# Performance work log

Hardware: AMD Instinct MI355X
Metric: run time of the kernel (lower is better)

## Reference

```python
import jax, jax.numpy as jnp
from jax import lax
import numpy as np


def setup_inputs() -> dict:
    key = jax.random.key(0)
    ks = iter(jax.random.split(key, 48))

    def w(shape):
        fan = shape[0] if len(shape) == 2 else int(np.prod(shape[1:]))
        return jax.random.normal(next(ks), shape, jnp.float32) / np.sqrt(fan)

    def b(n):
        return jax.random.normal(next(ks), (n,), jnp.float32) * 0.01

    T = 16
    return dict(
        search=jax.random.normal(next(ks), (3, 383, 287), jnp.float32),
        exemplars=jax.random.normal(next(ks), (T, 3, 383, 287), jnp.float32),
        # AlexNet features (random-weight stand-in for pretrained)
        aw1=w((64, 3, 11, 11)), ab1=b(64),
        aw2=w((192, 64, 5, 5)), ab2=b(192),
        aw3=w((384, 192, 3, 3)), ab3=b(384),
        aw4=w((256, 384, 3, 3)), ab4=b(256),
        aw5=w((256, 256, 3, 3)), ab5=b(256),
        # conv_deconv: Conv1d(256,256,3,p=1) -> MaxPool1d(88) -> ConvTranspose1d(256,256,88)
        wcd=w((256, 256, 3)), bcd=b(256),
        wt=w((256, 256, 88)), bt=b(256),
        # st_gcn: GCN(256, 512, 256)
        ws1=w((256, 512)), bs1=b(512),
        ws2=w((512, 256)), bs2=b(256),
        # g, h: 1x1 Conv1d(256,256) == linear maps
        wg=w((256, 256)), bg=b(256),
        wh=w((256, 256)), bh=b(256),
        # ct_gcn: GCN(256, 384, 256)
        wc1=w((256, 384)), bc1=b(384),
        wc2=w((384, 256)), bc2=b(256),
    )


def _gct_forward(search, exemplars, aw1, ab1, aw2, ab2, aw3, ab3, aw4, ab4,
                 aw5, ab5, wcd, bcd, wt, bt, ws1, bs1, ws2, bs2,
                 wg, bg, wh, bh, wc1, bc1, wc2, bc2):
    f32 = jnp.float32

    def conv2d(x, w, bias, s, p):
        y = lax.conv_general_dilated(x, w, (s, s), [(p, p), (p, p)],
                                     dimension_numbers=('NCHW', 'OIHW', 'NCHW'))
        return y + bias[None, :, None, None]

    def maxpool(x):  # k=3, s=2, VALID (AlexNet pools)
        return lax.reduce_window(x, -jnp.inf, lax.max, (1, 1, 3, 3), (1, 1, 2, 2), 'VALID')

    def features(x):
        x = maxpool(jax.nn.relu(conv2d(x, aw1, ab1, 4, 2)))
        x = maxpool(jax.nn.relu(conv2d(x, aw2, ab2, 1, 2)))
        x = jax.nn.relu(conv2d(x, aw3, ab3, 1, 1))
        x = jax.nn.relu(conv2d(x, aw4, ab4, 1, 1))
        x = maxpool(jax.nn.relu(conv2d(x, aw5, ab5, 1, 1)))
        return x

    lrelu = lambda v: jax.nn.leaky_relu(v, 0.01)

    X = features(search[None])          # [1,256,11,8]
    Z = features(exemplars)             # [T,256,11,8]
    T = Z.shape[0]
    D = X.shape[1]                      # 256
    M = X.shape[2] * X.shape[3]         # 88
    Xf = X.reshape(D, M)                # [256,88]
    Zf = Z.reshape(T, D, M)             # [T,256,88]

    # conv_deconv branch: conv1d(k=3,p=1) -> global maxpool -> conv_transpose(k=M)
    xc = lax.conv_general_dilated(Xf[None], wcd, (1,), [(1, 1)],
                                  dimension_numbers=('NCH', 'OIH', 'NCH'))[0] + bcd[:, None]
    v = jnp.max(xc, axis=1)                              # [256]
    X_hat = jnp.einsum('i,iok->ok', v, wt) + bt[:, None]  # [256,88]

    # spatiotemporal graph: A[i+T*j, i+T*k]=1 for j!=k; self-loops for t!=0
    TM = T * M
    n = jnp.arange(TM)
    same_t = (n[:, None] % T) == (n[None, :] % T)
    diff_s = (n[:, None] // T) != (n[None, :] // T)
    A1 = (same_t & diff_s).astype(f32) + jnp.diag((n % T != 0).astype(f32))

    # st GCN over TM nodes (node n = t + T*m -> spatial-major flatten)
    nodes = Zf.transpose(2, 0, 1).reshape(TM, D)          # [TM,256]
    h1 = lrelu(A1 @ (nodes @ ws1) + bs1)                  # [TM,512]
    h2 = lrelu(A1 @ (h1 @ ws2) + bs2)                     # [TM,256]
    V1 = jnp.max(h2.reshape(M, T, D), axis=1).T           # temporal max-pool -> [256,88]

    # dynamic cross-track graph: pairwise g/h affinities + row softmax (fused)
    Vx = V1 + X_hat                                       # [256,88]
    G = wg @ Vx + bg[:, None]                             # [256,88]
    Hh = wh @ Vx + bh[:, None]                            # [256,88]
    A2 = jax.nn.softmax(Hh.T @ G, axis=1)                 # [88,88], A2[j,i]=g(i).h(j)

    # ct GCN
    xv = V1.T                                             # [88,256]
    c1 = lrelu(A2 @ (xv @ wc1) + bc1)                     # [88,384]
    V2 = lrelu(A2 @ (c1 @ wc2) + bc2).T                   # [256,88]

    # F.conv2d(X[1,256,11,8], V2[1,256,11,8]) -> full-overlap correlation = scalar
    R = jnp.sum(Xf * V2).reshape(1, 1, 1, 1)
    return R


def reference(search, exemplars, aw1, ab1, aw2, ab2, aw3, ab3, aw4, ab4,
              aw5, ab5, wcd, bcd, wt, bt, ws1, bs1, ws2, bs2,
              wg, bg, wh, bh, wc1, bc1, wc2, bc2):
    return _gct_forward(search, exemplars, aw1, ab1, aw2, ab2, aw3, ab3, aw4, ab4,
                        aw5, ab5, wcd, bcd, wt, bt, ws1, bs1, ws2, bs2,
                        wg, bg, wh, bh, wc1, bc1, wc2, bc2)
```

## Files before the change

kernel.cpp:

```cpp
#include <hip/hip_runtime.h>
#include <hip/hip_bf16.h>
#include <math.h>

#define BATCH 17
#define T_EX 16
#define H0 383
#define W0 287
#define C1 64
#define H1 95
#define W1 71
#define H1P 47
#define W1P 35
#define C2 192
#define H2P 23
#define W2P 17
#define C3 384
#define C45 256
#define H5P 11
#define W5P 8
#define DD 256
#define MM 88
#define TM 1408

#define HP1 389
#define WP1 292

typedef unsigned short ushort_t;
typedef __attribute__((ext_vector_type(8))) short short8;
typedef __attribute__((ext_vector_type(4))) float f32x4;

__device__ __forceinline__ float lrelu(float v) { return v > 0.f ? v : 0.01f * v; }

__device__ __forceinline__ ushort_t f2bf(float f) {
    unsigned int u = __float_as_uint(f);
    unsigned int r = (u + 0x7fffu + ((u >> 16) & 1u)) >> 16;
    return (ushort_t)r;
}
__device__ __forceinline__ float b2f(ushort_t b) {
    return __uint_as_float(((unsigned int)b) << 16);
}
__device__ __forceinline__ short8 ld16(const ushort_t* p) { return *(const short8*)p; }
__device__ __forceinline__ short8 ld2x8(const ushort_t* p) {
    union { uint2 u[2]; short8 s; } uu;
    uu.u[0] = *(const uint2*)p;
    uu.u[1] = *(const uint2*)(p + 4);
    return uu.s;
}
__device__ __forceinline__ void async_cp16(ushort_t* l, const ushort_t* g) {
    __builtin_amdgcn_global_load_lds(
        (const __attribute__((address_space(1))) void*)g,
        (__attribute__((address_space(3))) void*)l, 16, 0, 0);
}

__global__ void zfill_k(float4* __restrict__ p, int n4) {
    int idx = blockIdx.x * 256 + threadIdx.x;
    if (idx < n4) p[idx] = (float4){0.f, 0.f, 0.f, 0.f};
}

__global__ void prep1_k(const float* __restrict__ search, const float* __restrict__ exemp,
                        ushort_t* __restrict__ out) {
    int idx = blockIdx.x * 256 + threadIdx.x;
    if (idx >= BATCH * H0 * W0) return;
    int ix = idx % W0; int t = idx / W0;
    int iy = t % H0; int b = t / H0;
    const float* src = (b == 0) ? search : exemp + (size_t)(b - 1) * 3 * H0 * W0;
    const int hw = H0 * W0;
    float v0 = src[iy * W0 + ix];
    float v1 = src[hw + iy * W0 + ix];
    float v2 = src[2 * hw + iy * W0 + ix];
    ushort4 o;
    o.x = f2bf(v0); o.y = f2bf(v1); o.z = f2bf(v2); o.w = 0;
    *(ushort4*)&out[(((size_t)b * HP1 + iy + 2) * WP1 + ix + 2) * 4] = o;
}

__global__ void wprep_k(const float* __restrict__ w, ushort_t* __restrict__ out,
                        int KH, int KWl, int KWr, int CINl, int CINr,
                        int NKS, int nch, int OCr) {
    int idx = blockIdx.x * 256 + threadIdx.x;
    if (idx >= nch) return;
    int c = idx & 255;
    int rest = idx >> 8;
    int ks = rest % NKS;
    int ocb = rest / NKS;
    int k8 = c >> 6, m = c & 63;
    int oc = ocb * 64 + m;
    int KWC = KWl * CINl;
    ushort_t* o = out + (size_t)idx * 8;
#pragma unroll
    for (int j = 0; j < 8; ++j) {
        int kg = ks * 32 + k8 * 8 + j;
        int ky = kg / KWC; int rem = kg - ky * KWC;
        int kx = rem / CINl; int ic = rem - kx * CINl;
        float v = 0.f;
        if (oc < OCr && ky < KH && kx < KWr && ic < CINr)
            v = w[(((size_t)oc * CINr + ic) * KH + ky) * KWr + kx];
        o[j] = f2bf(v);
    }
}

__global__ void wprep_gemm_k(const float* __restrict__ ws1, const float* __restrict__ ws2,
                             const float* __restrict__ wcd, ushort_t* __restrict__ WS1T,
                             ushort_t* __restrict__ WS2T, ushort_t* __restrict__ WCDT) {
    int idx = blockIdx.x * 256 + threadIdx.x;
    const float* src; ushort_t* dst; int NKS, mode = 0, sa = 1, sk = 0, base;
    if (idx < 16384)       { src = ws1; dst = WS1T; NKS = 8;  sk = 512; base = idx; }
    else if (idx < 32768)  { src = ws2; dst = WS2T; NKS = 16; sk = 256; base = idx - 16384; }
    else if (idx < 57344)  { src = wcd; dst = WCDT; NKS = 24; mode = 1; base = idx - 32768; }
    else return;
    int c = base & 255;
    int rest = base >> 8;
    int ks = rest % NKS;
    int ocb = rest / NKS;
    int k8 = c >> 6, m = c & 63;
    int oc = ocb * 64 + m;
    ushort_t* o = dst + (size_t)base * 8;
#pragma unroll
    for (int j = 0; j < 8; ++j) {
        int kg = ks * 32 + k8 * 8 + j;
        float v;
        if (mode == 0) v = src[(size_t)oc * sa + (size_t)kg * sk];
        else           v = src[(size_t)oc * 768 + (kg & 255) * 3 + (kg >> 8)];
        o[j] = f2bf(v);
    }
}

template <int STRIDE, bool A16>
__global__ __launch_bounds__(256) void conv_mfma13(
    const ushort_t* __restrict__ inp, const ushort_t* __restrict__ wt,
    const float* __restrict__ bias, ushort_t* __restrict__ out,
    int Hp, int Wp, int C, int Wout, int HW, int NKS2, int KWl,
    int OHp, int OWp, int OPAD, int COUT) {
    const int tid = threadIdx.x;
    const int wv = tid >> 6, lane = tid & 63;
    const int quad = lane >> 4, l16 = lane & 15;
    const int n_blk = blockIdx.x * 64;
    const int ocb = blockIdx.y;
    const int b = blockIdx.z;

    __shared__ ushort_t As[2][4096];
    __shared__ ushort_t Bs[2][4096];
    __shared__ int offs[432];

    const int KWC = KWl * C;
    for (int g = tid; g < NKS2 * 8; g += 256) {
        int kg = g * 8;
        int ky = kg / KWC; int rem = kg - ky * KWC;
        int kx = rem / C; int c8 = rem - kx * C;
        offs[g] = (ky * Wp + kx) * C + c8;
    }

    const ushort_t* inb = inp + (size_t)b * Hp * Wp * C;

    const int g8 = lane & 7, po = lane >> 3;
    int np0 = n_blk + wv * 16 + po;      if (np0 >= HW) np0 = HW - 1;
    int np1 = n_blk + wv * 16 + 8 + po;  if (np1 >= HW) np1 = HW - 1;
    const ushort_t* bsrc0;
    const ushort_t* bsrc1;
    {
        int oy0 = np0 / Wout, ox0 = np0 - oy0 * Wout;
        int oy1 = np1 / Wout, ox1 = np1 - oy1 * Wout;
        bsrc0 = inb + (size_t)(oy0 * STRIDE * Wp + ox0 * STRIDE) * C;
        bsrc1 = inb + (size_t)(oy1 * STRIDE * Wp + ox1 * STRIDE) * C;
    }
    const int ws0 = g8 * 512 + (((wv * 16 + po) ^ g8) * 8);
    const int ws1 = g8 * 512 + (((wv * 16 + 8 + po) ^ g8) * 8);

    int n_g = n_blk + lane;
    int n_gc = n_g < HW ? n_g : HW - 1;
    int oyl = n_gc / Wout, oxl = n_gc - oyl * Wout;
    const int base0 = (oyl * STRIDE * Wp + oxl * STRIDE) * C;

    f32x4 acc[4];
#pragma unroll
    for (int cn = 0; cn < 4; ++cn) acc[cn] = (f32x4){0.f, 0.f, 0.f, 0.f};

    const ushort_t* wblk = wt + (size_t)ocb * (size_t)NKS2 * 4096;

    __syncthreads();

    {
        const ushort_t* aS = wblk + tid * 8;
        async_cp16(&As[0][tid * 8], aS);
        async_cp16(&As[0][2048 + tid * 8], aS + 2048);
        if constexpr (A16) {
            short8 r0v = ld16(bsrc0 + offs[g8]);
            short8 r1v = ld16(bsrc1 + offs[g8]);
            *(short8*)&Bs[0][ws0] = r0v;
            *(short8*)&Bs[0][ws1] = r1v;
        } else {
            const int o0 = offs[wv], o1 = offs[4 + wv];
            *(short8*)&Bs[0][tid * 8] = ld2x8(inb + base0 + o0);
            *(short8*)&Bs[0][2048 + tid * 8] = ld2x8(inb + base0 + o1);
        }
    }
    __syncthreads();

    for (int ks2 = 0; ks2 < NKS2; ++ks2) {
        const int cur = ks2 & 1, nxt = cur ^ 1;
        const bool more = (ks2 + 1 < NKS2);
        short8 rb0, rb1;
        if (more) {
            const ushort_t* aS = wblk + (size_t)(ks2 + 1) * 4096 + tid * 8;
            async_cp16(&As[nxt][tid * 8], aS);
            async_cp16(&As[nxt][2048 + tid * 8], aS + 2048);
            if constexpr (A16) {
                rb0 = ld16(bsrc0 + offs[(ks2 + 1) * 8 + g8]);
                rb1 = ld16(bsrc1 + offs[(ks2 + 1) * 8 + g8]);
            } else {
                const int o0 = offs[(ks2 + 1) * 8 + wv], o1 = offs[(ks2 + 1) * 8 + 4 + wv];
                *(short8*)&Bs[nxt][tid * 8] = ld2x8(inb + base0 + o0);
                *(short8*)&Bs[nxt][2048 + tid * 8] = ld2x8(inb + base0 + o1);
            }
        }
#pragma unroll
        for (int h = 0; h < 2; ++h) {
            const short8 af = *(const short8*)&As[cur][h * 2048 + (quad * 64 + wv * 16 + l16) * 8];
#pragma unroll
            for (int cn = 0; cn < 4; ++cn) {
                int bidx;
                if constexpr (A16)
                    bidx = h * 2048 + quad * 512 + (((cn * 16 + l16) ^ (h * 4 + quad)) * 8);
                else
                    bidx = h * 2048 + (quad * 64 + cn * 16 + l16) * 8;
                const short8 bfr = *(const short8*)&Bs[cur][bidx];
                acc[cn] = __builtin_amdgcn_mfma_f32_16x16x32_bf16(af, bfr, acc[cn], 0, 0, 0);
            }
        }
        if constexpr (A16) {
            if (more) {
                *(short8*)&Bs[nxt][ws0] = rb0;
                *(short8*)&Bs[nxt][ws1] = rb1;
            }
        }
        __syncthreads();
    }

    const int oc0 = ocb * 64 + wv * 16 + quad * 4;
    const float bi0 = bias[oc0], bi1 = bias[oc0 + 1], bi2 = bias[oc0 + 2], bi3 = bias[oc0 + 3];
#pragma unroll
    for (int cn = 0; cn < 4; ++cn) {
        int n = n_blk + cn * 16 + l16;
        if (n < HW) {
            int y = n / Wout, x = n - y * Wout;
            size_t base = (((size_t)b * OHp + y + OPAD) * OWp + x + OPAD) * COUT + oc0;
            ushort4 o;
            o.x = f2bf(fmaxf(acc[cn][0] + bi0, 0.f));
            o.y = f2bf(fmaxf(acc[cn][1] + bi1, 0.f));
            o.z = f2bf(fmaxf(acc[cn][2] + bi2, 0.f));
            o.w = f2bf(fmaxf(acc[cn][3] + bi3, 0.f));
            *(ushort4*)&out[base] = o;
        }
    }
}

template <int MODE, bool HASBIAS, bool SC1>
__global__ __launch_bounds__(256) void gemm_mfma3(
    const ushort_t* __restrict__ Bsrc, const ushort_t* __restrict__ wt,
    const float* __restrict__ bias, float* __restrict__ out,
    int RS, int N, int NKS, int sn, int sc) {
    const int tid = threadIdx.x;
    const int wv = tid >> 6, lane = tid & 63;
    const int quad = lane >> 4, l16 = lane & 15;
    const int n_blk = blockIdx.x * 64;
    const int ocb = blockIdx.y;

    __shared__ ushort_t Bs[2][2048];

    int n_g = n_blk + lane;
    int n_gc = n_g < N ? n_g : N - 1;
    int row = (MODE == 1) ? (1 + (n_gc & 15)) * MM + (n_gc >> 4) : n_gc;
    const size_t base0 = (size_t)row * RS;

    f32x4 acc[4];
#pragma unroll
    for (int cn = 0; cn < 4; ++cn) acc[cn] = (f32x4){0.f, 0.f, 0.f, 0.f};

    const ushort_t* wblk = wt + (size_t)ocb * NKS * 2048;
    const int afrag = (quad * 64 + wv * 16 + l16) * 8;

    short8 a0 = ld16(wblk + afrag);
    *(short8*)&Bs[0][tid * 8] = ld16(Bsrc + base0 + wv * 8);
    __syncthreads();

    for (int ks = 0; ks < NKS; ++ks) {
        const int cur = ks & 1, nxt = cur ^ 1;
        short8 a1, bn;
        const bool more = (ks + 1 < NKS);
        if (more) {
            a1 = ld16(wblk + (ks + 1) * 2048 + afrag);
            bn = ld16(Bsrc + base0 + (ks + 1) * 32 + wv * 8);
        }
#pragma unroll
        for (int cn = 0; cn < 4; ++cn) {
            const short8 bfr = *(const short8*)&Bs[cur][(quad * 64 + cn * 16 + l16) * 8];
            acc[cn] = __builtin_amdgcn_mfma_f32_16x16x32_bf16(a0, bfr, acc[cn], 0, 0, 0);
        }
        if (more) *(short8*)&Bs[nxt][tid * 8] = bn;
        a0 = a1;
        __syncthreads();
    }

    const int oc0 = ocb * 64 + wv * 16 + quad * 4;
    float bb[4] = {0.f, 0.f, 0.f, 0.f};
    if (HASBIAS) { bb[0] = bias[oc0]; bb[1] = bias[oc0+1]; bb[2] = bias[oc0+2]; bb[3] = bias[oc0+3]; }
#pragma unroll
    for (int cn = 0; cn < 4; ++cn) {
        int n = n_blk + cn * 16 + l16;
        if (n < N) {
            if (SC1) {
                float4 o;
                o.x = acc[cn][0] + bb[0]; o.y = acc[cn][1] + bb[1];
                o.z = acc[cn][2] + bb[2]; o.w = acc[cn][3] + bb[3];
                *(float4*)&out[(size_t)n * sn + oc0] = o;
            } else {
#pragma unroll
                for (int reg = 0; reg < 4; ++reg)
                    out[(size_t)n * sn + (size_t)(oc0 + reg) * sc] = acc[cn][reg] + bb[reg];
            }
        }
    }
}

__global__ void pool_nhwc(const ushort_t* __restrict__ in, ushort_t* __restrict__ out,
                          int C, int Hin, int Win, int Hout, int Wout,
                          int OHp, int OWp, int OPAD) {
    int total = BATCH * C * Hout * Wout;
    int idx = blockIdx.x * 256 + threadIdx.x;
    if (idx >= total) return;
    int c = idx % C; int r = idx / C;
    int x = r % Wout; r /= Wout;
    int y = r % Hout; int b = r / Hout;
    const int rs = Win * C;
    const ushort_t* p = in + (((size_t)b * Hin + 2 * y) * Win + 2 * x) * C + c;
    float m = b2f(p[0]);
    m = fmaxf(m, b2f(p[C])); m = fmaxf(m, b2f(p[2 * C]));
    m = fmaxf(m, b2f(p[rs])); m = fmaxf(m, b2f(p[rs + C])); m = fmaxf(m, b2f(p[rs + 2 * C]));
    m = fmaxf(m, b2f(p[2 * rs])); m = fmaxf(m, b2f(p[2 * rs + C])); m = fmaxf(m, b2f(p[2 * rs + 2 * C]));
    out[(((size_t)b * OHp + y + OPAD) * OWp + x + OPAD) * C + c] = f2bf(m);
}

__global__ void pool5_k(const ushort_t* __restrict__ in, float* __restrict__ P,
                        ushort_t* __restrict__ PB, ushort_t* __restrict__ XfPad) {
    int total = BATCH * 256 * MM;
    int idx = blockIdx.x * 256 + threadIdx.x;
    if (idx >= total) return;
    int c = idx % 256; int r = idx / 256;
    int x = r % W5P; r /= W5P;
    int y = r % H5P; int b = r / H5P;
    const int rs = W2P * 256;
    const ushort_t* p = in + (((size_t)b * H2P + 2 * y) * W2P + 2 * x) * 256 + c;
    float m = b2f(p[0]);
    m = fmaxf(m, b2f(p[256])); m = fmaxf(m, b2f(p[512]));
    m = fmaxf(m, b2f(p[rs])); m = fmaxf(m, b2f(p[rs + 256])); m = fmaxf(m, b2f(p[rs + 512]));
    m = fmaxf(m, b2f(p[2 * rs])); m = fmaxf(m, b2f(p[2 * rs + 256])); m = fmaxf(m, b2f(p[2 * rs + 512]));
    int mm = y * W5P + x;
    size_t o = ((size_t)b * MM + mm) * 256 + c;
    P[o] = m;
    ushort_t mb = f2bf(m);
    PB[o] = mb;
    if (b == 0) XfPad[(size_t)(mm + 1) * 256 + c] = mb;
}

__global__ void xhat2_k(const float* __restrict__ xc, const float* __restrict__ wt,
                        const float* __restrict__ bt, float* __restrict__ xhat) {
    __shared__ float lv[256];
    {
        int j = threadIdx.x;
        const float* xr = xc + (size_t)j * MM;
        float mx = xr[0];
        for (int k = 1; k < MM; ++k) mx = fmaxf(mx, xr[k]);
        lv[j] = mx;
    }
    __syncthreads();
    int idx = blockIdx.x * 256 + threadIdx.x;
    if (idx >= DD * MM) return;
    int k = idx % MM, o = idx / MM;
    float acc = bt[o];
    for (int i = 0; i < 256; ++i) acc = fmaf(lv[i], wt[(i * 256 + o) * MM + k], acc);
    xhat[idx] = acc;
}

__global__ void sh1_k(const float* __restrict__ Y1, const float* __restrict__ bs1,
                      ushort_t* __restrict__ h1b) {
    int idx = blockIdx.x * 256 + threadIdx.x;
    if (idx >= T_EX * 512) return;
    int c = idx & 511, t = idx >> 9;
    float s = 0.f;
    for (int m = 0; m < MM; ++m) s += Y1[(size_t)(m * T_EX + t) * 512 + c];
    float base = s + bs1[c];
    if (t == 0) {
        for (int m = 0; m < MM; ++m) {
            float val = base - Y1[(size_t)(m * T_EX) * 512 + c];
            h1b[(size_t)(m * T_EX) * 512 + c] = f2bf(lrelu(val));
        }
    } else {
        ushort_t v = f2bf(lrelu(base));
        for (int m = 0; m < MM; ++m)
            h1b[(size_t)(m * T_EX + t) * 512 + c] = v;
    }
}

__global__ void sh2_k(const float* __restrict__ Y2, const float* __restrict__ bs2,
                      float* __restrict__ h2) {
    int idx = blockIdx.x * 256 + threadIdx.x;
    if (idx >= T_EX * 256) return;
    int c = idx & 255, t = idx >> 8;
    float s = 0.f;
    for (int m = 0; m < MM; ++m) s += Y2[(size_t)(m * T_EX + t) * 256 + c];
    float base = s + bs2[c];
    if (t == 0) {
        for (int m = 0; m < MM; ++m)
            h2[(size_t)(m * T_EX) * 256 + c] = lrelu(base - Y2[(size_t)(m * T_EX) * 256 + c]);
    } else {
        float v = lrelu(base);
        for (int m = 0; m < MM; ++m) h2[(size_t)(m * T_EX + t) * 256 + c] = v;
    }
}

__global__ void v1vx_k(const float* __restrict__ h2, const float* __restrict__ xhat,
                       float* __restrict__ V1, float* __restrict__ Vx) {
    int idx = blockIdx.x * 256 + threadIdx.x;
    if (idx >= DD * MM) return;
    int m = idx % MM, d = idx / MM;
    float mx = -INFINITY;
    for (int t = 0; t < T_EX; ++t) mx = fmaxf(mx, h2[(m * T_EX + t) * 256 + d]);
    V1[idx] = mx;
    Vx[idx] = mx + xhat[idx];
}

__global__ void lin88_k(const float* __restrict__ Wg, const float* __restrict__ bg,
                        const float* __restrict__ Wh, const float* __restrict__ bh,
                        const float* __restrict__ Vin, float* __restrict__ Gout,
                        float* __restrict__ Hout) {
    int idx = blockIdx.x * 256 + threadIdx.x;
    if (idx >= DD * MM) return;
    const float* W = blockIdx.y ? Wh : Wg;
    const float* bias = blockIdx.y ? bh : bg;
    float* out = blockIdx.y ? Hout : Gout;
    int m = idx % MM, o = idx / MM;
    const float* wr = W + o * 256;
    float acc = bias[o];
    for (int i = 0; i < 256; ++i) acc = fmaf(wr[i], Vin[i * MM + m], acc);
    out[idx] = acc;
}

__global__ void smsm_k(const float* __restrict__ Hh, const float* __restrict__ G,
                       float* __restrict__ A2) {
    int j = blockIdx.x;
    int tid = threadIdx.x;
    __shared__ float row[96];
    __shared__ float red[128];
    for (int i = tid; i < MM; i += 128) {
        float acc = 0.f;
        for (int c = 0; c < 256; ++c) acc = fmaf(Hh[c * MM + j], G[c * MM + i], acc);
        row[i] = acc;
    }
    __syncthreads();
    float val = (tid < MM) ? row[tid] : -INFINITY;
    red[tid] = val; __syncthreads();
    for (int s = 64; s > 0; s >>= 1) {
        if (tid < s) red[tid] = fmaxf(red[tid], red[tid + s]);
        __syncthreads();
    }
    float mx = red[0]; __syncthreads();
    float e = (tid < MM) ? expf(val - mx) : 0.f;
    red[tid] = e; __syncthreads();
    for (int s = 64; s > 0; s >>= 1) {
        if (tid < s) red[tid] += red[tid + s];
        __syncthreads();
    }
    float inv = 1.f / red[0];
    if (tid < MM) A2[j * MM + tid] = e * inv;
}

__global__ void t1_k(const float* __restrict__ V1, const float* __restrict__ wc1,
                     float* __restrict__ t1) {
    int idx = blockIdx.x * 256 + threadIdx.x;
    if (idx >= MM * 384) return;
    int c = idx % 384, m = idx / 384;
    float acc = 0.f;
    for (int d = 0; d < 256; ++d) acc = fmaf(V1[d * MM + m], wc1[d * 384 + c], acc);
    t1[idx] = acc;
}

__global__ void c1_k(const float* __restrict__ A2, const float* __restrict__ t1,
                     const float* __restrict__ bc1, float* __restrict__ c1) {
    int idx = blockIdx.x * 256 + threadIdx.x;
    if (idx >= MM * 384) return;
    int c = idx % 384, j = idx / 384;
    float acc = bc1[c];
    for (int i = 0; i < MM; ++i) acc = fmaf(A2[j * MM + i], t1[i * 384 + c], acc);
    c1[idx] = lrelu(acc);
}

__global__ void t2_k(const float* __restrict__ c1, const float* __restrict__ wc2,
                     float* __restrict__ t2) {
    int idx = blockIdx.x * 256 + threadIdx.x;
    if (idx >= MM * 256) return;
    int c = idx % 256, m = idx / 256;
    const float* cr = c1 + m * 384;
    float acc = 0.f;
    for (int d = 0; d < 384; ++d) acc = fmaf(cr[d], wc2[d * 256 + c], acc);
    t2[idx] = acc;
}

__global__ void v2_k(const float* __restrict__ A2, const float* __restrict__ t2,
                     const float* __restrict__ bc2, float* __restrict__ V2m) {
    int idx = blockIdx.x * 256 + threadIdx.x;
    if (idx >= MM * 256) return;
    int c = idx % 256, j = idx / 256;
    float acc = bc2[c];
    for (int i = 0; i < MM; ++i) acc = fmaf(A2[j * MM + i], t2[i * 256 + c], acc);
    V2m[idx] = lrelu(acc);
}

__global__ void final_k(const float* __restrict__ Xf2, const float* __restrict__ V2m,
                        float* __restrict__ out) {
    __shared__ float red[256];
    float acc = 0.f;
    for (int idx = threadIdx.x; idx < DD * MM; idx += 256)
        acc = fmaf(Xf2[idx], V2m[idx], acc);
    red[threadIdx.x] = acc; __syncthreads();
    for (int s = 128; s > 0; s >>= 1) {
        if (threadIdx.x < s) red[threadIdx.x] += red[threadIdx.x + s];
        __syncthreads();
    }
    if (threadIdx.x == 0) out[0] = red[0];
}

extern "C" void kernel_launch(void* const* d_in, const int* in_sizes, int n_in,
                              void* d_out, int out_size, void* d_ws, size_t ws_size,
                              hipStream_t stream) {
    const float* search = (const float*)d_in[0];
    const float* exemp  = (const float*)d_in[1];
    const float* aw1 = (const float*)d_in[2];  const float* ab1 = (const float*)d_in[3];
    const float* aw2 = (const float*)d_in[4];  const float* ab2 = (const float*)d_in[5];
    const float* aw3 = (const float*)d_in[6];  const float* ab3 = (const float*)d_in[7];
    const float* aw4 = (const float*)d_in[8];  const float* ab4 = (const float*)d_in[9];
    const float* aw5 = (const float*)d_in[10]; const float* ab5 = (const float*)d_in[11];
    const float* wcd = (const float*)d_in[12]; const float* bcd = (const float*)d_in[13];
    const float* wt  = (const float*)d_in[14]; const float* bt  = (const float*)d_in[15];
    const float* ws1 = (const float*)d_in[16]; const float* bs1 = (const float*)d_in[17];
    const float* ws2 = (const float*)d_in[18]; const float* bs2 = (const float*)d_in[19];
    const float* wg  = (const float*)d_in[20]; const float* bg  = (const float*)d_in[21];
    const float* wh  = (const float*)d_in[22]; const float* bh  = (const float*)d_in[23];
    const float* wc1 = (const float*)d_in[24]; const float* bc1 = (const float*)d_in[25];
    const float* wc2 = (const float*)d_in[26]; const float* bc2 = (const float*)d_in[27];

    float* ws = (float*)d_ws;
    float* R1 = ws;
    float* R2 = ws + 3870720;
    float* R3 = ws + 7544832;
    float* Wg = ws + 8628864;

    ushort_t* in1p  = (ushort_t*)R1;
    ushort_t* c1out = (ushort_t*)R2;
    ushort_t* p1out = (ushort_t*)R3;
    ushort_t* c2out = (ushort_t*)R1;
    ushort_t* p2out = (ushort_t*)R2;
    ushort_t* c3out = (ushort_t*)(R2 + 775200);
    ushort_t* c4out = (ushort_t*)R1;
    ushort_t* c5out = (ushort_t*)R3;
    ushort_t* WT    = (ushort_t*)Wg;

    zfill_k<<<(965500 + 255) / 256, 256, 0, stream>>>((float4*)R1, 965500);
    prep1_k<<<(BATCH * H0 * W0 + 255) / 256, 256, 0, stream>>>(search, exemp, in1p);
    wprep_k<<<(4608 + 255) / 256, 256, 0, stream>>>(aw1, WT, 11, 12, 11, 4, 3, 18, 4608, 64);
    conv_mfma13<4, false><<<dim3(106, 1, BATCH), 256, 0, stream>>>(
        in1p, WT, ab1, c1out, HP1, WP1, 4, W1, H1 * W1, 9, 12, H1, W1, 0, 64);
    zfill_k<<<(270504 + 255) / 256, 256, 0, stream>>>((float4*)R3, 270504);
    pool_nhwc<<<(BATCH * 64 * H1P * W1P + 255) / 256, 256, 0, stream>>>(
        c1out, p1out, 64, H1, W1, H1P, W1P, 51, 39, 2);
    wprep_k<<<(38400 + 255) / 256, 256, 0, stream>>>(aw2, WT, 5, 5, 5, 64, 64, 50, 38400, 192);
    conv_mfma13<1, true><<<dim3(26, 3, BATCH), 256, 0, stream>>>(
        p1out, WT, ab2, c2out, 51, 39, 64, W1P, H1P * W1P, 25, 5, H1P, W1P, 0, 192);
    zfill_k<<<(581400 + 255) / 256, 256, 0, stream>>>((float4*)R2, 581400);
    pool_nhwc<<<(BATCH * 192 * H2P * W2P + 255) / 256, 256, 0, stream>>>(
        c2out, p2out, 192, H1P, W1P, H2P, W2P, 25, 19, 1);
    wprep_k<<<(82944 + 255) / 256, 256, 0, stream>>>(aw3, WT, 3, 3, 3, 192, 192, 54, 82944, 384);
    conv_mfma13<1, true><<<dim3(7, 6, BATCH), 256, 0, stream>>>(
        p2out, WT, ab3, c3out, 25, 19, 192, W2P, H2P * W2P, 27, 3, 25, 19, 1, 384);
    zfill_k<<<(258400 + 255) / 256, 256, 0, stream>>>((float4*)R1, 258400);
    wprep_k<<<(110592 + 255) / 256, 256, 0, stream>>>(aw4, WT, 3, 3, 3, 384, 384, 108, 110592, 256);
    conv_mfma13<1, true><<<dim3(7, 4, BATCH), 256, 0, stream>>>(
        c3out, WT, ab4, c4out, 25, 19, 384, W2P, H2P * W2P, 54, 3, 25, 19, 1, 256);
    wprep_k<<<(73728 + 255) / 256, 256, 0, stream>>>(aw5, WT, 3, 3, 3, 256, 256, 72, 73728, 256);
    conv_mfma13<1, true><<<dim3(7, 4, BATCH), 256, 0, stream>>>(
        c4out, WT, ab5, c5out, 25, 19, 256, W2P, H2P * W2P, 36, 3, H2P, W2P, 0, 256);

    float*    P      = R1 + 2417664;
    ushort_t* PB     = (ushort_t*)(R1 + 2800640);
    ushort_t* XfPad  = (ushort_t*)(R1 + 2992128);
    float*    xc     = R1 + 3003648;

    ushort_t* WS1T = (ushort_t*)Wg;
    ushort_t* WS2T = (ushort_t*)(Wg + 65536);
    ushort_t* WCDT = (ushort_t*)(Wg + 131072);
    wprep_gemm_k<<<(57344 + 255) / 256, 256, 0, stream>>>(ws1, ws2, wcd, WS1T, WS2T, WCDT);

    pool5_k<<<(BATCH * 256 * MM + 255) / 256, 256, 0, stream>>>(c5out, P, PB, XfPad);
    float* Xf2 = P;

    float* xhat = R1 + 1024;
    float* Y1   = R1 + 23552;
    ushort_t* h1b = (ushort_t*)(R1 + 752640);
    float* Y2   = R1 + 1473536;
    float* h2   = R1 + 1838080;
    float* V1   = R1 + 2198528;
    float* Vx   = R1 + 2221056;
    float* G    = R1 + 2243584;
    float* Hh   = R1 + 2266112;
    float* A2   = R1 + 2296832;
    float* t1   = R1 + 2305024;
    float* c1   = R1 + 2338816;
    float* t2   = R1 + 2372608;
    float* V2m  = R1 + 2395136;

    gemm_mfma3<0, true, false><<<dim3(2, 4), 256, 0, stream>>>(
        XfPad, WCDT, bcd, xc, 256, MM, 24, 1, MM);
    xhat2_k<<<(DD * MM + 255) / 256, 256, 0, stream>>>(xc, wt, bt, xhat);

    gemm_mfma3<1, false, true><<<dim3(22, 8), 256, 0, stream>>>(
        PB, WS1T, nullptr, Y1, 256, TM, 8, 512, 1);
    sh1_k<<<(T_EX * 512 + 255) / 256, 256, 0, stream>>>(Y1, bs1, h1b);
    gemm_mfma3<0, false, true><<<dim3(22, 4), 256, 0, stream>>>(
        h1b, WS2T, nullptr, Y2, 512, TM, 16, 256, 1);
    sh2_k<<<(T_EX * 256 + 255) / 256, 256, 0, stream>>>(Y2, bs2, h2);
    v1vx_k<<<(DD * MM + 255) / 256, 256, 0, stream>>>(h2, xhat, V1, Vx);

    lin88_k<<<dim3((DD * MM + 255) / 256, 2), 256, 0, stream>>>(wg, bg, wh, bh, Vx, G, Hh);
    smsm_k<<<MM, 128, 0, stream>>>(Hh, G, A2);

    t1_k<<<(MM * 384 + 255) / 256, 256, 0, stream>>>(V1, wc1, t1);
    c1_k<<<(MM * 384 + 255) / 256, 256, 0, stream>>>(A2, t1, bc1, c1);
    t2_k<<<(MM * 256 + 255) / 256, 256, 0, stream>>>(c1, wc2, t2);
    v2_k<<<(MM * 256 + 255) / 256, 256, 0, stream>>>(A2, t2, bc2, V2m);

    final_k<<<1, 256, 0, stream>>>(Xf2, V2m, (float*)d_out);
}
```

Measured before the change: 548.2 us.

## Fold batch into conv N dimension, 2x2 wave tiling, and merge small kernels

The conv kernel now flattens batch and pixels into one N dimension, so tiles no longer waste work on per-image remainders, and each wave computes a 32x32 output sub-tile with 2x2 MFMAs instead of 16x64. Zero-fill passes are removed: the input prep writes its own padding, and the remaining fills are folded into pool and weight-prep launches. Several small GEMM and elementwise kernels are merged into combined launches (gemm pair, xhat+sh1, lin+t1, wprep+pool5). This cuts launch count and idle tile work, at the cost of more divergent multi-role kernels and different register pressure.

```diff
diff --git a/kernel.cpp b/kernel.cpp
--- a/kernel.cpp
+++ b/kernel.cpp
@@ -52,30 +52,34 @@
         (__attribute__((address_space(3))) void*)l, 16, 0, 0);
 }
 
-__global__ void zfill_k(float4* __restrict__ p, int n4) {
-    int idx = blockIdx.x * 256 + threadIdx.x;
-    if (idx < n4) p[idx] = (float4){0.f, 0.f, 0.f, 0.f};
-}
-
-__global__ void prep1_k(const float* __restrict__ search, const float* __restrict__ exemp,
-                        ushort_t* __restrict__ out) {
-    int idx = blockIdx.x * 256 + threadIdx.x;
-    if (idx >= BATCH * H0 * W0) return;
-    int ix = idx % W0; int t = idx / W0;
-    int iy = t % H0; int b = t / H0;
-    const float* src = (b == 0) ? search : exemp + (size_t)(b - 1) * 3 * H0 * W0;
-    const int hw = H0 * W0;
-    float v0 = src[iy * W0 + ix];
-    float v1 = src[hw + iy * W0 + ix];
-    float v2 = src[2 * hw + iy * W0 + ix];
-    ushort4 o;
-    o.x = f2bf(v0); o.y = f2bf(v1); o.z = f2bf(v2); o.w = 0;
-    *(ushort4*)&out[(((size_t)b * HP1 + iy + 2) * WP1 + ix + 2) * 4] = o;
+__global__ void prep1f_k(const float* __restrict__ search, const float* __restrict__ exemp,
+                         ushort_t* __restrict__ out) {
+    int idx = blockIdx.x * 256 + threadIdx.x;
+    if (idx >= BATCH * HP1 * WP1) return;
+    int x = idx % WP1; int t = idx / WP1;
+    int y = t % HP1; int b = t / HP1;
+    ushort4 o = {0, 0, 0, 0};
+    int ix = x - 2, iy = y - 2;
+    if (ix >= 0 && ix < W0 && iy >= 0 && iy < H0) {
+        const float* src = (b == 0) ? search : exemp + (size_t)(b - 1) * 3 * H0 * W0;
+        const int hw = H0 * W0;
+        o.x = f2bf(src[iy * W0 + ix]);
+        o.y = f2bf(src[hw + iy * W0 + ix]);
+        o.z = f2bf(src[2 * hw + iy * W0 + ix]);
+    }
+    *(ushort4*)&out[(size_t)idx * 4] = o;
 }
 
 __global__ void wprep_k(const float* __restrict__ w, ushort_t* __restrict__ out,
                         int KH, int KWl, int KWr, int CINl, int CINr,
-                        int NKS, int nch, int OCr) {
+                        int NKS, int nch, int OCr,
+                        float4* __restrict__ zp, int zn4) {
+    const int wb = (nch + 255) >> 8;
+    if ((int)blockIdx.x >= wb) {
+        int z = (blockIdx.x - wb) * 256 + threadIdx.x;
+        if (z < zn4) zp[z] = (float4){0.f, 0.f, 0.f, 0.f};
+        return;
+    }
     int idx = blockIdx.x * 256 + threadIdx.x;
     if (idx >= nch) return;
     int c = idx & 255;
@@ -98,44 +102,18 @@
     }
 }
 
-__global__ void wprep_gemm_k(const float* __restrict__ ws1, const float* __restrict__ ws2,
-                             const float* __restrict__ wcd, ushort_t* __restrict__ WS1T,
-                             ushort_t* __restrict__ WS2T, ushort_t* __restrict__ WCDT) {
-    int idx = blockIdx.x * 256 + threadIdx.x;
-    const float* src; ushort_t* dst; int NKS, mode = 0, sa = 1, sk = 0, base;
-    if (idx < 16384)       { src = ws1; dst = WS1T; NKS = 8;  sk = 512; base = idx; }
-    else if (idx < 32768)  { src = ws2; dst = WS2T; NKS = 16; sk = 256; base = idx - 16384; }
-    else if (idx < 57344)  { src = wcd; dst = WCDT; NKS = 24; mode = 1; base = idx - 32768; }
-    else return;
-    int c = base & 255;
-    int rest = base >> 8;
-    int ks = rest % NKS;
-    int ocb = rest / NKS;
-    int k8 = c >> 6, m = c & 63;
-    int oc = ocb * 64 + m;
-    ushort_t* o = dst + (size_t)base * 8;
-#pragma unroll
-    for (int j = 0; j < 8; ++j) {
-        int kg = ks * 32 + k8 * 8 + j;
-        float v;
-        if (mode == 0) v = src[(size_t)oc * sa + (size_t)kg * sk];
-        else           v = src[(size_t)oc * 768 + (kg & 255) * 3 + (kg >> 8)];
-        o[j] = f2bf(v);
-    }
-}
-
 template <int STRIDE, bool A16>
-__global__ __launch_bounds__(256) void conv_mfma13(
+__global__ __launch_bounds__(256) void conv_mfma14(
     const ushort_t* __restrict__ inp, const ushort_t* __restrict__ wt,
     const float* __restrict__ bias, ushort_t* __restrict__ out,
-    int Hp, int Wp, int C, int Wout, int HW, int NKS2, int KWl,
+    int Hp, int Wp, int C, int Wout, int HW, int Ntot, int NKS2, int KWl,
     int OHp, int OWp, int OPAD, int COUT) {
     const int tid = threadIdx.x;
     const int wv = tid >> 6, lane = tid & 63;
     const int quad = lane >> 4, l16 = lane & 15;
+    const int wr = wv >> 1, wc = wv & 1;
     const int n_blk = blockIdx.x * 64;
     const int ocb = blockIdx.y;
-    const int b = blockIdx.z;
 
     __shared__ ushort_t As[2][4096];
     __shared__ ushort_t Bs[2][4096];
@@ -149,30 +127,35 @@
         offs[g] = (ky * Wp + kx) * C + c8;
     }
 
-    const ushort_t* inb = inp + (size_t)b * Hp * Wp * C;
+    const size_t HWC = (size_t)Hp * Wp * C;
 
     const int g8 = lane & 7, po = lane >> 3;
-    int np0 = n_blk + wv * 16 + po;      if (np0 >= HW) np0 = HW - 1;
-    int np1 = n_blk + wv * 16 + 8 + po;  if (np1 >= HW) np1 = HW - 1;
-    const ushort_t* bsrc0;
-    const ushort_t* bsrc1;
-    {
-        int oy0 = np0 / Wout, ox0 = np0 - oy0 * Wout;
-        int oy1 = np1 / Wout, ox1 = np1 - oy1 * Wout;
-        bsrc0 = inb + (size_t)(oy0 * STRIDE * Wp + ox0 * STRIDE) * C;
-        bsrc1 = inb + (size_t)(oy1 * STRIDE * Wp + ox1 * STRIDE) * C;
-    }
-    const int ws0 = g8 * 512 + (((wv * 16 + po) ^ g8) * 8);
-    const int ws1 = g8 * 512 + (((wv * 16 + 8 + po) ^ g8) * 8);
-
-    int n_g = n_blk + lane;
-    int n_gc = n_g < HW ? n_g : HW - 1;
-    int oyl = n_gc / Wout, oxl = n_gc - oyl * Wout;
-    const int base0 = (oyl * STRIDE * Wp + oxl * STRIDE) * C;
-
-    f32x4 acc[4];
-#pragma unroll
-    for (int cn = 0; cn < 4; ++cn) acc[cn] = (f32x4){0.f, 0.f, 0.f, 0.f};
+    const ushort_t* bsrc0 = nullptr; const ushort_t* bsrc1 = nullptr;
+    const ushort_t* lsrc = nullptr;
+    int ws0 = 0, ws1 = 0;
+    if constexpr (A16) {
+        int np0 = n_blk + wv * 16 + po;      if (np0 >= Ntot) np0 = Ntot - 1;
+        int np1 = n_blk + wv * 16 + 8 + po;  if (np1 >= Ntot) np1 = Ntot - 1;
+        int b0 = np0 / HW, p0 = np0 - b0 * HW;
+        int b1 = np1 / HW, p1 = np1 - b1 * HW;
+        int oy0 = p0 / Wout, ox0 = p0 - oy0 * Wout;
+        int oy1 = p1 / Wout, ox1 = p1 - oy1 * Wout;
+        bsrc0 = inp + (size_t)b0 * HWC + (size_t)(oy0 * STRIDE * Wp + ox0 * STRIDE) * C;
+        bsrc1 = inp + (size_t)b1 * HWC + (size_t)(oy1 * STRIDE * Wp + ox1 * STRIDE) * C;
+        ws0 = g8 * 512 + (((wv * 16 + po) ^ g8) * 8);
+        ws1 = g8 * 512 + (((wv * 16 + 8 + po) ^ g8) * 8);
+    } else {
+        int n0 = n_blk + lane; if (n0 >= Ntot) n0 = Ntot - 1;
+        int b0 = n0 / HW, p0 = n0 - b0 * HW;
+        int oy = p0 / Wout, ox = p0 - oy * Wout;
+        lsrc = inp + (size_t)b0 * HWC + (size_t)(oy * STRIDE * Wp + ox * STRIDE) * C;
+    }
+
+    f32x4 acc[2][2];
+#pragma unroll
+    for (int am = 0; am < 2; ++am)
+#pragma unroll
+        for (int bn = 0; bn < 2; ++bn) acc[am][bn] = (f32x4){0.f, 0.f, 0.f, 0.f};
 
     const ushort_t* wblk = wt + (size_t)ocb * (size_t)NKS2 * 4096;
 
@@ -183,14 +166,12 @@
         async_cp16(&As[0][tid * 8], aS);
         async_cp16(&As[0][2048 + tid * 8], aS + 2048);
         if constexpr (A16) {
-            short8 r0v = ld16(bsrc0 + offs[g8]);
-            short8 r1v = ld16(bsrc1 + offs[g8]);
-            *(short8*)&Bs[0][ws0] = r0v;
-            *(short8*)&Bs[0][ws1] = r1v;
+            *(short8*)&Bs[0][ws0] = ld16(bsrc0 + offs[g8]);
+            *(short8*)&Bs[0][ws1] = ld16(bsrc1 + offs[g8]);
         } else {
             const int o0 = offs[wv], o1 = offs[4 + wv];
-            *(short8*)&Bs[0][tid * 8] = ld2x8(inb + base0 + o0);
-            *(short8*)&Bs[0][2048 + tid * 8] = ld2x8(inb + base0 + o1);
+            *(short8*)&Bs[0][tid * 8] = ld2x8(lsrc + o0);
+            *(short8*)&Bs[0][2048 + tid * 8] = ld2x8(lsrc + o1);
         }
     }
     __syncthreads();
@@ -208,23 +189,26 @@
                 rb1 = ld16(bsrc1 + offs[(ks2 + 1) * 8 + g8]);
             } else {
                 const int o0 = offs[(ks2 + 1) * 8 + wv], o1 = offs[(ks2 + 1) * 8 + 4 + wv];
-                *(short8*)&Bs[nxt][tid * 8] = ld2x8(inb + base0 + o0);
-                *(short8*)&Bs[nxt][2048 + tid * 8] = ld2x8(inb + base0 + o1);
+                *(short8*)&Bs[nxt][tid * 8] = ld2x8(lsrc + o0);
+                *(short8*)&Bs[nxt][2048 + tid * 8] = ld2x8(lsrc + o1);
             }
         }
 #pragma unroll
         for (int h = 0; h < 2; ++h) {
-            const short8 af = *(const short8*)&As[cur][h * 2048 + (quad * 64 + wv * 16 + l16) * 8];
-#pragma unroll
-            for (int cn = 0; cn < 4; ++cn) {
-                int bidx;
-                if constexpr (A16)
-                    bidx = h * 2048 + quad * 512 + (((cn * 16 + l16) ^ (h * 4 + quad)) * 8);
-                else
-                    bidx = h * 2048 + (quad * 64 + cn * 16 + l16) * 8;
-                const short8 bfr = *(const short8*)&Bs[cur][bidx];
-                acc[cn] = __builtin_amdgcn_mfma_f32_16x16x32_bf16(af, bfr, acc[cn], 0, 0, 0);
+            const short8 a0 = *(const short8*)&As[cur][h * 2048 + (quad * 64 + wr * 32 + l16) * 8];
+            const short8 a1 = *(const short8*)&As[cur][h * 2048 + (quad * 64 + wr * 32 + 16 + l16) * 8];
+            short8 b0, b1;
+            if constexpr (A16) {
+                b0 = *(const short8*)&Bs[cur][h * 2048 + quad * 512 + (((wc * 32 + l16) ^ (h * 4 + quad)) * 8)];
+                b1 = *(const short8*)&Bs[cur][h * 2048 + quad * 512 + (((wc * 32 + 16 + l16) ^ (h * 4 + quad)) * 8)];
+            } else {
+                b0 = *(const short8*)&Bs[cur][h * 2048 + (quad * 64 + wc * 32 + l16) * 8];
+                b1 = *(const short8*)&Bs[cur][h * 2048 + (quad * 64 + wc * 32 + 16 + l16) * 8];
             }
+            acc[0][0] = __builtin_amdgcn_mfma_f32_16x16x32_bf16(a0, b0, acc[0][0], 0, 0, 0);
+            acc[0][1] = __builtin_amdgcn_mfma_f32_16x16x32_bf16(a0, b1, acc[0][1], 0, 0, 0);
+            acc[1][0] = __builtin_amdgcn_mfma_f32_16x16x32_bf16(a1, b0, acc[1][0], 0, 0, 0);
+            acc[1][1] = __builtin_amdgcn_mfma_f32_16x16x32_bf16(a1, b1, acc[1][1], 0, 0, 0);
         }
         if constexpr (A16) {
             if (more) {
@@ -235,36 +219,39 @@
         __syncthreads();
     }
 
-    const int oc0 = ocb * 64 + wv * 16 + quad * 4;
-    const float bi0 = bias[oc0], bi1 = bias[oc0 + 1], bi2 = bias[oc0 + 2], bi3 = bias[oc0 + 3];
-#pragma unroll
-    for (int cn = 0; cn < 4; ++cn) {
-        int n = n_blk + cn * 16 + l16;
-        if (n < HW) {
-            int y = n / Wout, x = n - y * Wout;
-            size_t base = (((size_t)b * OHp + y + OPAD) * OWp + x + OPAD) * COUT + oc0;
-            ushort4 o;
-            o.x = f2bf(fmaxf(acc[cn][0] + bi0, 0.f));
-            o.y = f2bf(fmaxf(acc[cn][1] + bi1, 0.f));
-            o.z = f2bf(fmaxf(acc[cn][2] + bi2, 0.f));
-            o.w = f2bf(fmaxf(acc[cn][3] + bi3, 0.f));
-            *(ushort4*)&out[base] = o;
+    const int oc0 = ocb * 64 + wr * 32 + quad * 4;
+#pragma unroll
+    for (int bn = 0; bn < 2; ++bn) {
+        int n = n_blk + wc * 32 + bn * 16 + l16;
+        if (n < Ntot) {
+            int bb = n / HW; int pix = n - bb * HW;
+            int y = pix / Wout, x = pix - y * Wout;
+            size_t base = (((size_t)bb * OHp + y + OPAD) * OWp + x + OPAD) * COUT;
+#pragma unroll
+            for (int am = 0; am < 2; ++am) {
+                const int oc = oc0 + am * 16;
+                ushort4 o;
+                o.x = f2bf(fmaxf(acc[am][bn][0] + bias[oc], 0.f));
+                o.y = f2bf(fmaxf(acc[am][bn][1] + bias[oc + 1], 0.f));
+                o.z = f2bf(fmaxf(acc[am][bn][2] + bias[oc + 2], 0.f));
+                o.w = f2bf(fmaxf(acc[am][bn][3] + bias[oc + 3], 0.f));
+                *(ushort4*)&out[base + oc] = o;
+            }
         }
     }
 }
 
 template <int MODE, bool HASBIAS, bool SC1>
-__global__ __launch_bounds__(256) void gemm_mfma3(
+__device__ __forceinline__ void gemm_dev(
+    ushort_t (*Bs)[2048],
     const ushort_t* __restrict__ Bsrc, const ushort_t* __restrict__ wt,
     const float* __restrict__ bias, float* __restrict__ out,
-    int RS, int N, int NKS, int sn, int sc) {
+    int RS, int N, int NKS, int sn, int sc, int bx, int by) {
     const int tid = threadIdx.x;
     const int wv = tid >> 6, lane = tid & 63;
     const int quad = lane >> 4, l16 = lane & 15;
-    const int n_blk = blockIdx.x * 64;
-    const int ocb = blockIdx.y;
-
-    __shared__ ushort_t Bs[2][2048];
+    const int n_blk = bx * 64;
+    const int ocb = by;
 
     int n_g = n_blk + lane;
     int n_gc = n_g < N ? n_g : N - 1;
@@ -321,82 +308,146 @@
     }
 }
 
-__global__ void pool_nhwc(const ushort_t* __restrict__ in, ushort_t* __restrict__ out,
-                          int C, int Hin, int Win, int Hout, int Wout,
-                          int OHp, int OWp, int OPAD) {
-    int total = BATCH * C * Hout * Wout;
+template <int MODE, bool HASBIAS, bool SC1>
+__global__ __launch_bounds__(256) void gemm_mfma3_k(
+    const ushort_t* __restrict__ Bsrc, const ushort_t* __restrict__ wt,
+    const float* __restrict__ bias, float* __restrict__ out,
+    int RS, int N, int NKS, int sn, int sc) {
+    __shared__ ushort_t Bs[2][2048];
+    gemm_dev<MODE, HASBIAS, SC1>(Bs, Bsrc, wt, bias, out, RS, N, NKS, sn, sc,
+                                 blockIdx.x, blockIdx.y);
+}
+
+__global__ __launch_bounds__(256) void gemm_pair_k(
+    const ushort_t* __restrict__ XfPad, const ushort_t* __restrict__ WCDT,
+    const float* __restrict__ bcd, float* __restrict__ xc,
+    const ushort_t* __restrict__ PB, const ushort_t* __restrict__ WS1T,
+    float* __restrict__ Y1) {
+    __shared__ ushort_t Bs[2][2048];
+    if (blockIdx.x < 2) {
+        if (blockIdx.y < 4)
+            gemm_dev<0, true, false>(Bs, XfPad, WCDT, bcd, xc, 256, MM, 24, 1, MM,
+                                     blockIdx.x, blockIdx.y);
+    } else {
+        gemm_dev<1, false, true>(Bs, PB, WS1T, nullptr, Y1, 256, TM, 8, 512, 1,
+                                 blockIdx.x - 2, blockIdx.y);
+    }
+}
+
+__global__ void pool_p_k(const ushort_t* __restrict__ in, ushort_t* __restrict__ out,
+                         int C, int Hin, int Win, int Hout, int Wout,
+                         int OHp, int OWp, int OPAD,
+                         float4* __restrict__ zp, int zn4) {
+    const int total = BATCH * C * OHp * OWp;
+    const int pb = (total + 255) >> 8;
+    if ((int)blockIdx.x >= pb) {
+        int z = (blockIdx.x - pb) * 256 + threadIdx.x;
+        if (z < zn4) zp[z] = (float4){0.f, 0.f, 0.f, 0.f};
+        return;
+    }
     int idx = blockIdx.x * 256 + threadIdx.x;
     if (idx >= total) return;
     int c = idx % C; int r = idx / C;
-    int x = r % Wout; r /= Wout;
-    int y = r % Hout; int b = r / Hout;
-    const int rs = Win * C;
-    const ushort_t* p = in + (((size_t)b * Hin + 2 * y) * Win + 2 * x) * C + c;
-    float m = b2f(p[0]);
-    m = fmaxf(m, b2f(p[C])); m = fmaxf(m, b2f(p[2 * C]));
-    m = fmaxf(m, b2f(p[rs])); m = fmaxf(m, b2f(p[rs + C])); m = fmaxf(m, b2f(p[rs + 2 * C]));
-    m = fmaxf(m, b2f(p[2 * rs])); m = fmaxf(m, b2f(p[2 * rs + C])); m = fmaxf(m, b2f(p[2 * rs + 2 * C]));
-    out[(((size_t)b * OHp + y + OPAD) * OWp + x + OPAD) * C + c] = f2bf(m);
-}
-
-__global__ void pool5_k(const ushort_t* __restrict__ in, float* __restrict__ P,
-                        ushort_t* __restrict__ PB, ushort_t* __restrict__ XfPad) {
-    int total = BATCH * 256 * MM;
-    int idx = blockIdx.x * 256 + threadIdx.x;
-    if (idx >= total) return;
-    int c = idx % 256; int r = idx / 256;
-    int x = r % W5P; r /= W5P;
-    int y = r % H5P; int b = r / H5P;
-    const int rs = W2P * 256;
-    const ushort_t* p = in + (((size_t)b * H2P + 2 * y) * W2P + 2 * x) * 256 + c;
-    float m = b2f(p[0]);
-    m = fmaxf(m, b2f(p[256])); m = fmaxf(m, b2f(p[512]));
-    m = fmaxf(m, b2f(p[rs])); m = fmaxf(m, b2f(p[rs + 256])); m = fmaxf(m, b2f(p[rs + 512]));
-    m = fmaxf(m, b2f(p[2 * rs])); m = fmaxf(m, b2f(p[2 * rs + 256])); m = fmaxf(m, b2f(p[2 * rs + 512]));
-    int mm = y * W5P + x;
-    size_t o = ((size_t)b * MM + mm) * 256 + c;
-    P[o] = m;
-    ushort_t mb = f2bf(m);
-    PB[o] = mb;
-    if (b == 0) XfPad[(size_t)(mm + 1) * 256 + c] = mb;
-}
-
-__global__ void xhat2_k(const float* __restrict__ xc, const float* __restrict__ wt,
-                        const float* __restrict__ bt, float* __restrict__ xhat) {
-    __shared__ float lv[256];
-    {
-        int j = threadIdx.x;
-        const float* xr = xc + (size_t)j * MM;
-        float mx = xr[0];
-        for (int k = 1; k < MM; ++k) mx = fmaxf(mx, xr[k]);
-        lv[j] = mx;
-    }
-    __syncthreads();
-    int idx = blockIdx.x * 256 + threadIdx.x;
-    if (idx >= DD * MM) return;
-    int k = idx % MM, o = idx / MM;
-    float acc = bt[o];
-    for (int i = 0; i < 256; ++i) acc = fmaf(lv[i], wt[(i * 256 + o) * MM + k], acc);
-    xhat[idx] = acc;
-}
-
-__global__ void sh1_k(const float* __restrict__ Y1, const float* __restrict__ bs1,
-                      ushort_t* __restrict__ h1b) {
-    int idx = blockIdx.x * 256 + threadIdx.x;
-    if (idx >= T_EX * 512) return;
-    int c = idx & 511, t = idx >> 9;
-    float s = 0.f;
-    for (int m = 0; m < MM; ++m) s += Y1[(size_t)(m * T_EX + t) * 512 + c];
-    float base = s + bs1[c];
-    if (t == 0) {
-        for (int m = 0; m < MM; ++m) {
-            float val = base - Y1[(size_t)(m * T_EX) * 512 + c];
-            h1b[(size_t)(m * T_EX) * 512 + c] = f2bf(lrelu(val));
+    int x = r % OWp; r /= OWp;
+    int y = r % OHp; int b = r / OHp;
+    int iy = y - OPAD, ix = x - OPAD;
+    ushort_t v = 0;
+    if (iy >= 0 && iy < Hout && ix >= 0 && ix < Wout) {
+        const int rs = Win * C;
+        const ushort_t* p = in + (((size_t)b * Hin + 2 * iy) * Win + 2 * ix) * C + c;
+        float m = b2f(p[0]);
+        m = fmaxf(m, b2f(p[C])); m = fmaxf(m, b2f(p[2 * C]));
+        m = fmaxf(m, b2f(p[rs])); m = fmaxf(m, b2f(p[rs + C])); m = fmaxf(m, b2f(p[rs + 2 * C]));
+        m = fmaxf(m, b2f(p[2 * rs])); m = fmaxf(m, b2f(p[2 * rs + C])); m = fmaxf(m, b2f(p[2 * rs + 2 * C]));
+        v = f2bf(m);
+    }
+    out[idx] = v;
+}
+
+__global__ void wg_pool5_k(const float* __restrict__ ws1, const float* __restrict__ ws2,
+                           const float* __restrict__ wcd, ushort_t* __restrict__ WS1T,
+                           ushort_t* __restrict__ WS2T, ushort_t* __restrict__ WCDT,
+                           const ushort_t* __restrict__ in, float* __restrict__ P,
+                           ushort_t* __restrict__ PB, ushort_t* __restrict__ XfPad) {
+    if (blockIdx.x < 224) {
+        int idx = blockIdx.x * 256 + threadIdx.x;
+        const float* src; ushort_t* dst; int NKS, mode = 0, sa = 1, sk = 0, base;
+        if (idx < 16384)       { src = ws1; dst = WS1T; NKS = 8;  sk = 512; base = idx; }
+        else if (idx < 32768)  { src = ws2; dst = WS2T; NKS = 16; sk = 256; base = idx - 16384; }
+        else                   { src = wcd; dst = WCDT; NKS = 24; mode = 1; base = idx - 32768; }
+        int c = base & 255;
+        int rest = base >> 8;
+        int ks = rest % NKS;
+        int ocb = rest / NKS;
+        int k8 = c >> 6, m = c & 63;
+        int oc = ocb * 64 + m;
+        ushort_t* o = dst + (size_t)base * 8;
+#pragma unroll
+        for (int j = 0; j < 8; ++j) {
+            int kg = ks * 32 + k8 * 8 + j;
+            float v;
+            if (mode == 0) v = src[(size_t)oc * sa + (size_t)kg * sk];
+            else           v = src[(size_t)oc * 768 + (kg & 255) * 3 + (kg >> 8)];
+            o[j] = f2bf(v);
         }
     } else {
-        ushort_t v = f2bf(lrelu(base));
-        for (int m = 0; m < MM; ++m)
-            h1b[(size_t)(m * T_EX + t) * 512 + c] = v;
+        int idx = (blockIdx.x - 224) * 256 + threadIdx.x;
+        if (idx >= BATCH * 256 * MM) return;
+        int c = idx % 256; int r = idx / 256;
+        int x = r % W5P; r /= W5P;
+        int y = r % H5P; int b = r / H5P;
+        const int rs = W2P * 256;
+        const ushort_t* p = in + (((size_t)b * H2P + 2 * y) * W2P + 2 * x) * 256 + c;
+        float m = b2f(p[0]);
+        m = fmaxf(m, b2f(p[256])); m = fmaxf(m, b2f(p[512]));
+        m = fmaxf(m, b2f(p[rs])); m = fmaxf(m, b2f(p[rs + 256])); m = fmaxf(m, b2f(p[rs + 512]));
+        m = fmaxf(m, b2f(p[2 * rs])); m = fmaxf(m, b2f(p[2 * rs + 256])); m = fmaxf(m, b2f(p[2 * rs + 512]));
+        int mm = y * W5P + x;
+        size_t o = ((size_t)b * MM + mm) * 256 + c;
+        P[o] = m;
+        ushort_t mb = f2bf(m);
+        PB[o] = mb;
+        if (b == 0) XfPad[(size_t)(mm + 1) * 256 + c] = mb;
+    }
+}
+
+__global__ void xhat_sh1_k(const float* __restrict__ xc, const float* __restrict__ wt,
+                           const float* __restrict__ bt, float* __restrict__ xhat,
+                           const float* __restrict__ Y1, const float* __restrict__ bs1,
+                           ushort_t* __restrict__ h1b) {
+    if (blockIdx.x < 88) {
+        __shared__ float lv[256];
+        {
+            int j = threadIdx.x;
+            const float* xr = xc + (size_t)j * MM;
+            float mx = xr[0];
+            for (int k = 1; k < MM; ++k) mx = fmaxf(mx, xr[k]);
+            lv[j] = mx;
+        }
+        __syncthreads();
+        int idx = blockIdx.x * 256 + threadIdx.x;
+        if (idx >= DD * MM) return;
+        int k = idx % MM, o = idx / MM;
+        float acc = bt[o];
+        for (int i = 0; i < 256; ++i) acc = fmaf(lv[i], wt[(i * 256 + o) * MM + k], acc);
+        xhat[idx] = acc;
+    } else {
+        int idx = (blockIdx.x - 88) * 256 + threadIdx.x;
+        if (idx >= T_EX * 512) return;
+        int c = idx & 511, t = idx >> 9;
+        float s = 0.f;
+        for (int m = 0; m < MM; ++m) s += Y1[(size_t)(m * T_EX + t) * 512 + c];
+        float base = s + bs1[c];
+        if (t == 0) {
+            for (int m = 0; m < MM; ++m) {
+                float val = base - Y1[(size_t)(m * T_EX) * 512 + c];
+                h1b[(size_t)(m * T_EX) * 512 + c] = f2bf(lrelu(val));
+            }
+        } else {
+            ushort_t v = f2bf(lrelu(base));
+            for (int m = 0; m < MM; ++m)
+                h1b[(size_t)(m * T_EX + t) * 512 + c] = v;
+        }
     }
 }
 
@@ -428,20 +479,33 @@
     Vx[idx] = mx + xhat[idx];
 }
 
-__global__ void lin88_k(const float* __restrict__ Wg, const float* __restrict__ bg,
-                        const float* __restrict__ Wh, const float* __restrict__ bh,
-                        const float* __restrict__ Vin, float* __restrict__ Gout,
-                        float* __restrict__ Hout) {
-    int idx = blockIdx.x * 256 + threadIdx.x;
-    if (idx >= DD * MM) return;
-    const float* W = blockIdx.y ? Wh : Wg;
-    const float* bias = blockIdx.y ? bh : bg;
-    float* out = blockIdx.y ? Hout : Gout;
-    int m = idx % MM, o = idx / MM;
-    const float* wr = W + o * 256;
-    float acc = bias[o];
-    for (int i = 0; i < 256; ++i) acc = fmaf(wr[i], Vin[i * MM + m], acc);
-    out[idx] = acc;
+__global__ void lin_t1_k(const float* __restrict__ Wgm, const float* __restrict__ bg,
+                         const float* __restrict__ Whm, const float* __restrict__ bh,
+                         const float* __restrict__ Vx, float* __restrict__ G,
+                         float* __restrict__ Hh,
+                         const float* __restrict__ V1, const float* __restrict__ wc1,
+                         float* __restrict__ t1) {
+    int bx = blockIdx.x;
+    if (bx < 176) {
+        int sel = bx >= 88;
+        int idx = (bx - (sel ? 88 : 0)) * 256 + threadIdx.x;
+        if (idx >= DD * MM) return;
+        const float* W = sel ? Whm : Wgm;
+        const float* bias = sel ? bh : bg;
+        float* out = sel ? Hh : G;
+        int m = idx % MM, o = idx / MM;
+        const float* wr = W + o * 256;
+        float acc = bias[o];
+        for (int i = 0; i < 256; ++i) acc = fmaf(wr[i], Vx[i * MM + m], acc);
+        out[idx] = acc;
+    } else {
+        int idx = (bx - 176) * 256 + threadIdx.x;
+        if (idx >= MM * 384) return;
+        int c = idx % 384, m = idx / 384;
+        float acc = 0.f;
+        for (int d = 0; d < 256; ++d) acc = fmaf(V1[d * MM + m], wc1[d * 384 + c], acc);
+        t1[idx] = acc;
+    }
 }
 
 __global__ void smsm_k(const float* __restrict__ Hh, const float* __restrict__ G,
@@ -471,16 +535,6 @@
     }
     float inv = 1.f / red[0];
     if (tid < MM) A2[j * MM + tid] = e * inv;
-}
-
-__global__ void t1_k(const float* __restrict__ V1, const float* __restrict__ wc1,
-                     float* __restrict__ t1) {
-    int idx = blockIdx.x * 256 + threadIdx.x;
-    if (idx >= MM * 384) return;
-    int c = idx % 384, m = idx / 384;
-    float acc = 0.f;
-    for (int d = 0; d < 256; ++d) acc = fmaf(V1[d * MM + m], wc1[d * 384 + c], acc);
-    t1[idx] = acc;
 }
 
 __global__ void c1_k(const float* __restrict__ A2, const float* __restrict__ t1,
@@ -563,30 +617,27 @@
     ushort_t* c5out = (ushort_t*)R3;
     ushort_t* WT    = (ushort_t*)Wg;
 
-    zfill_k<<<(965500 + 255) / 256, 256, 0, stream>>>((float4*)R1, 965500);
-    prep1_k<<<(BATCH * H0 * W0 + 255) / 256, 256, 0, stream>>>(search, exemp, in1p);
-    wprep_k<<<(4608 + 255) / 256, 256, 0, stream>>>(aw1, WT, 11, 12, 11, 4, 3, 18, 4608, 64);
-    conv_mfma13<4, false><<<dim3(106, 1, BATCH), 256, 0, stream>>>(
-        in1p, WT, ab1, c1out, HP1, WP1, 4, W1, H1 * W1, 9, 12, H1, W1, 0, 64);
-    zfill_k<<<(270504 + 255) / 256, 256, 0, stream>>>((float4*)R3, 270504);
-    pool_nhwc<<<(BATCH * 64 * H1P * W1P + 255) / 256, 256, 0, stream>>>(
-        c1out, p1out, 64, H1, W1, H1P, W1P, 51, 39, 2);
-    wprep_k<<<(38400 + 255) / 256, 256, 0, stream>>>(aw2, WT, 5, 5, 5, 64, 64, 50, 38400, 192);
-    conv_mfma13<1, true><<<dim3(26, 3, BATCH), 256, 0, stream>>>(
-        p1out, WT, ab2, c2out, 51, 39, 64, W1P, H1P * W1P, 25, 5, H1P, W1P, 0, 192);
-    zfill_k<<<(581400 + 255) / 256, 256, 0, stream>>>((float4*)R2, 581400);
-    pool_nhwc<<<(BATCH * 192 * H2P * W2P + 255) / 256, 256, 0, stream>>>(
-        c2out, p2out, 192, H1P, W1P, H2P, W2P, 25, 19, 1);
-    wprep_k<<<(82944 + 255) / 256, 256, 0, stream>>>(aw3, WT, 3, 3, 3, 192, 192, 54, 82944, 384);
-    conv_mfma13<1, true><<<dim3(7, 6, BATCH), 256, 0, stream>>>(
-        p2out, WT, ab3, c3out, 25, 19, 192, W2P, H2P * W2P, 27, 3, 25, 19, 1, 384);
-    zfill_k<<<(258400 + 255) / 256, 256, 0, stream>>>((float4*)R1, 258400);
-    wprep_k<<<(110592 + 255) / 256, 256, 0, stream>>>(aw4, WT, 3, 3, 3, 384, 384, 108, 110592, 256);
-    conv_mfma13<1, true><<<dim3(7, 4, BATCH), 256, 0, stream>>>(
-        c3out, WT, ab4, c4out, 25, 19, 384, W2P, H2P * W2P, 54, 3, 25, 19, 1, 256);
-    wprep_k<<<(73728 + 255) / 256, 256, 0, stream>>>(aw5, WT, 3, 3, 3, 256, 256, 72, 73728, 256);
-    conv_mfma13<1, true><<<dim3(7, 4, BATCH), 256, 0, stream>>>(
-        c4out, WT, ab5, c5out, 25, 19, 256, W2P, H2P * W2P, 36, 3, H2P, W2P, 0, 256);
+    prep1f_k<<<(BATCH * HP1 * WP1 + 255) / 256, 256, 0, stream>>>(search, exemp, in1p);
+    wprep_k<<<18, 256, 0, stream>>>(aw1, WT, 11, 12, 11, 4, 3, 18, 4608, 64, nullptr, 0);
+    conv_mfma14<4, false><<<dim3(1792, 1), 256, 0, stream>>>(
+        in1p, WT, ab1, c1out, HP1, WP1, 4, W1, H1 * W1, BATCH * H1 * W1, 9, 12, H1, W1, 0, 64);
+    pool_p_k<<<(BATCH * 64 * 51 * 39 + 255) / 256, 256, 0, stream>>>(
+        c1out, p1out, 64, H1, W1, H1P, W1P, 51, 39, 2, nullptr, 0);
+    wprep_k<<<150, 256, 0, stream>>>(aw2, WT, 5, 5, 5, 64, 64, 50, 38400, 192, nullptr, 0);
+    conv_mfma14<1, true><<<dim3(437, 3), 256, 0, stream>>>(
+        p1out, WT, ab2, c2out, 51, 39, 64, W1P, H1P * W1P, BATCH * H1P * W1P, 25, 5, H1P, W1P, 0, 192);
+    pool_p_k<<<(BATCH * 192 * 25 * 19 + 255) / 256 + 1515, 256, 0, stream>>>(
+        c2out, p2out, 192, H1P, W1P, H2P, W2P, 25, 19, 1, (float4*)(R2 + 775200), 387600);
+    wprep_k<<<324, 256, 0, stream>>>(aw3, WT, 3, 3, 3, 192, 192, 54, 82944, 384, nullptr, 0);
+    conv_mfma14<1, true><<<dim3(104, 6), 256, 0, stream>>>(
+        p2out, WT, ab3, c3out, 25, 19, 192, W2P, H2P * W2P, BATCH * H2P * W2P, 27, 3, 25, 19, 1, 384);
+    wprep_k<<<432 + 1010, 256, 0, stream>>>(aw4, WT, 3, 3, 3, 384, 384, 108, 110592, 256,
+                                            (float4*)R1, 258400);
+    conv_mfma14<1, true><<<dim3(104, 4), 256, 0, stream>>>(
+        c3out, WT, ab4, c4out, 25, 19, 384, W2P, H2P * W2P, BATCH * H2P * W2P, 54, 3, 25, 19, 1, 256);
+    wprep_k<<<288, 256, 0, stream>>>(aw5, WT, 3, 3, 3, 256, 256, 72, 73728, 256, nullptr, 0);
+    conv_mfma14<1, true><<<dim3(104, 4), 256, 0, stream>>>(
+        c4out, WT, ab5, c5out, 25, 19, 256, W2P, H2P * W2P, BATCH * H2P * W2P, 36, 3, H2P, W2P, 0, 256);
 
     float*    P      = R1 + 2417664;
     ushort_t* PB     = (ushort_t*)(R1 + 2800640);
@@ -596,9 +647,9 @@
     ushort_t* WS1T = (ushort_t*)Wg;
     ushort_t* WS2T = (ushort_t*)(Wg + 65536);
     ushort_t* WCDT = (ushort_t*)(Wg + 131072);
-    wprep_gemm_k<<<(57344 + 255) / 256, 256, 0, stream>>>(ws1, ws2, wcd, WS1T, WS2T, WCDT);
-
-    pool5_k<<<(BATCH * 256 * MM + 255) / 256, 256, 0, stream>>>(c5out, P, PB, XfPad);
+
+    wg_pool5_k<<<224 + (BATCH * 256 * MM + 255) / 256, 256, 0, stream>>>(
+        ws1, ws2, wcd, WS1T, WS2T, WCDT, c5out, P, PB, XfPad);
     float* Xf2 = P;
 
     float* xhat = R1 + 1024;
@@ -616,22 +667,17 @@
     float* t2   = R1 + 2372608;
     float* V2m  = R1 + 2395136;
 
-    gemm_mfma3<0, true, false><<<dim3(2, 4), 256, 0, stream>>>(
-        XfPad, WCDT, bcd, xc, 256, MM, 24, 1, MM);
-    xhat2_k<<<(DD * MM + 255) / 256, 256, 0, stream>>>(xc, wt, bt, xhat);
-
-    gemm_mfma3<1, false, true><<<dim3(22, 8), 256, 0, stream>>>(
-        PB, WS1T, nullptr, Y1, 256, TM, 8, 512, 1);
-    sh1_k<<<(T_EX * 512 + 255) / 256, 256, 0, stream>>>(Y1, bs1, h1b);
-    gemm_mfma3<0, false, true><<<dim3(22, 4), 256, 0, stream>>>(
+    gemm_pair_k<<<dim3(24, 8), 256, 0, stream>>>(XfPad, WCDT, bcd, xc, PB, WS1T, Y1);
+    xhat_sh1_k<<<120, 256, 0, stream>>>(xc, wt, bt, xhat, Y1, bs1, h1b);
+
+    gemm_mfma3_k<0, false, true><<<dim3(22, 4), 256, 0, stream>>>(
         h1b, WS2T, nullptr, Y2, 512, TM, 16, 256, 1);
     sh2_k<<<(T_EX * 256 + 255) / 256, 256, 0, stream>>>(Y2, bs2, h2);
     v1vx_k<<<(DD * MM + 255) / 256, 256, 0, stream>>>(h2, xhat, V1, Vx);
 
-    lin88_k<<<dim3((DD * MM + 255) / 256, 2), 256, 0, stream>>>(wg, bg, wh, bh, Vx, G, Hh);
+    lin_t1_k<<<308, 256, 0, stream>>>(wg, bg, wh, bh, Vx, G, Hh, V1, wc1, t1);
     smsm_k<<<MM, 128, 0, stream>>>(Hh, G, A2);
 
-    t1_k<<<(MM * 384 + 255) / 256, 256, 0, stream>>>(V1, wc1, t1);
     c1_k<<<(MM * 384 + 255) / 256, 256, 0, stream>>>(A2, t1, bc1, c1);
     t2_k<<<(MM * 256 + 255) / 256, 256, 0, stream>>>(c1, wc2, t2);
     v2_k<<<(MM * 256 + 255) / 256, 256, 0, stream>>>(A2, t2, bc2, V2m);
```

Result: faster. 477.2 us (-12.9%).
